# Optimization experiments

Measured on AMD Instinct MI355X. Metric: run time of the kernel, lower is better.

Reference implementation:

```python
import jax, jax.numpy as jnp
import numpy as np

EPS = 1e-5

def _bn(x):
    # BatchNorm (training-mode batch stats, gamma=1, beta=0) over batch+spatial axes
    axes = (0,) + tuple(range(2, x.ndim))
    m = x.mean(axis=axes, keepdims=True)
    v = x.var(axis=axes, keepdims=True)
    return (x - m) / jnp.sqrt(v + EPS)

def _knn(x, k):
    # x: [B, C, N] -> idx [B, N, K] of k nearest neighbors (largest of negative sq dist)
    xt = jnp.swapaxes(x, 1, 2)                      # [B, N, C]
    inner = -2.0 * jnp.einsum('bnc,bmc->bnm', xt, xt)
    xx = jnp.sum(x * x, axis=1)                     # [B, N]
    pdist = -xx[:, :, None] - inner - xx[:, None, :]  # [B, N, N] (negative sq dist)
    return jax.lax.top_k(pdist, k)[1]

def _get_neighbors(x, k):
    # x: [B, C, N] -> edge features [B, 2C, N, K] = concat(neighbor - center, center)
    idx = _knn(x, k)                                # [B, N, K]
    xt = jnp.swapaxes(x, 1, 2)                      # [B, N, C]
    nb = jax.vmap(lambda pts, i: pts[i])(xt, idx)   # [B, N, K, C]
    center = jnp.broadcast_to(xt[:, :, None, :], nb.shape)
    feat = jnp.concatenate([nb - center, center], axis=-1)  # [B, N, K, 2C]
    return jnp.transpose(feat, (0, 3, 1, 2))        # [B, 2C, N, K]

def _sa_layer(x, Wq, Wk, Wt, bt):
    # Faithful SALayerSingleHead: note original computes x_v but never uses it,
    # and uses x @ attention; we match that math exactly. x: [B, C, N]
    xq = jnp.einsum('qc,bcn->bnq', Wq, x)           # [B, N, C/4]
    xk = jnp.einsum('qc,bcn->bqn', Wk, x)           # [B, C/4, N]
    energy = jnp.einsum('bnq,bqm->bnm', xq, xk)     # [B, N, N]
    attn = jax.nn.softmax(energy, axis=-1)
    attn = attn / (1e-6 + attn.sum(axis=1, keepdims=True))
    xr = jnp.einsum('bcn,bnm->bcm', x, attn)        # [B, C, N]
    xr = jax.nn.relu(_bn(jnp.einsum('oc,bcn->bon', Wt, x - xr) + bt[None, :, None]))
    return x + xr

def setup_inputs() -> dict:
    key = jax.random.key(0)
    ks = jax.random.split(key, 12)
    B, N, K = 8, 2048, 32
    s = 0.02
    inp = {
        'x': jax.random.normal(ks[0], (B, 3, N), dtype=jnp.float32),
        'We1': jax.random.normal(ks[1], (64, 6), dtype=jnp.float32) * s,
        'be1': jnp.zeros((64,), jnp.float32),
        'We2': jax.random.normal(ks[2], (64, 128), dtype=jnp.float32) * s,
        'be2': jnp.zeros((64,), jnp.float32),
        'Wq': jax.random.normal(ks[3], (4, 32, 128), dtype=jnp.float32) * s,
        'Wk': jax.random.normal(ks[4], (4, 32, 128), dtype=jnp.float32) * s,
        'Wt': jax.random.normal(ks[5], (4, 128, 128), dtype=jnp.float32) * s,
        'bt': jnp.zeros((4, 128), jnp.float32),
        'Wf': jax.random.normal(ks[6], (1024, 512), dtype=jnp.float32) * s,
        'bf': jnp.zeros((1024,), jnp.float32),
        'Wc1': jax.random.normal(ks[7], (512, 1536), dtype=jnp.float32) * s,
        'bc1': jnp.zeros((512,), jnp.float32),
        'Wc2': jax.random.normal(ks[8], (256, 512), dtype=jnp.float32) * s,
        'bc2': jnp.zeros((256,), jnp.float32),
        'Wc3': jax.random.normal(ks[9], (13, 256), dtype=jnp.float32) * s,
        'bc3': jnp.zeros((13,), jnp.float32),
        'k': K,
    }
    return inp

def reference(x, We1, be1, We2, be2, Wq, Wk, Wt, bt, Wf, bf, Wc1, bc1, Wc2, bc2, Wc3, bc3, k):
    # EdgeConv block 1: xyz -> 64
    e1 = jnp.einsum('oc,bcnk->bonk', We1, _get_neighbors(x, k)) + be1[None, :, None, None]
    f1 = jax.nn.relu(_bn(e1)).max(axis=-1)          # [B, 64, N]
    # EdgeConv block 2: 64 -> 64
    e2 = jnp.einsum('oc,bcnk->bonk', We2, _get_neighbors(f1, k)) + be2[None, :, None, None]
    f2 = jax.nn.relu(_bn(e2)).max(axis=-1)          # [B, 64, N]
    feat = jnp.concatenate([f1, f2], axis=1)        # [B, 128, N]
    # 4 stacked single-head SA layers (PCT offset attention)
    xs = feat
    outs = []
    for i in range(4):
        xs = _sa_layer(xs, Wq[i], Wk[i], Wt[i], bt[i])
        outs.append(xs)
    cat = jnp.concatenate(outs, axis=1)             # [B, 512, N]
    fuse = jax.nn.relu(_bn(jnp.einsum('oc,bcn->bon', Wf, cat) + bf[None, :, None]))  # [B,1024,N]
    g = fuse.max(axis=-1)                           # [B, 1024]
    gl = jnp.broadcast_to(g[:, :, None], (g.shape[0], g.shape[1], cat.shape[2]))
    h = jnp.concatenate([gl, cat], axis=1)          # [B, 1536, N]
    h = jax.nn.relu(_bn(jnp.einsum('oc,bcn->bon', Wc1, h) + bc1[None, :, None]))
    h = jax.nn.relu(_bn(jnp.einsum('oc,bcn->bon', Wc2, h) + bc2[None, :, None]))
    out = jnp.einsum('oc,bcn->bon', Wc3, h) + bc3[None, :, None]  # [B, 13, N]
    return out
```

## Files before the change

### kernel.cpp

```cpp
#include <hip/hip_runtime.h>
#include <math.h>

#define DEV static __device__ __forceinline__

namespace {

constexpr int B = 8;
constexpr int N = 2048;
constexpr int KNN = 32;
constexpr float BNEPS = 1e-5f;

DEV unsigned f2key(float f) {
  unsigned u = __float_as_uint(f);
  return (u & 0x80000000u) ? ~u : (u | 0x80000000u);
}

DEV void atomicMaxFloat(float* addr, float val) {
  if (val >= 0.0f) atomicMax((int*)addr, __float_as_int(val));
  else atomicMin((unsigned int*)addr, (unsigned int)__float_as_int(val));
}

struct SelScratch {
  unsigned hist[256];
  int ss[257];
  int bin;
  int cnt;
};

template <int NK>
DEV unsigned long long radix_select32(const unsigned long long (&keys)[NK], SelScratch& s) {
  const int t = threadIdx.x;
  const int lane = t & 63, wave = t >> 6;
  unsigned long long prefix = 0; unsigned long long T = 0;
  int needed = KNN;
  bool done = false;
  for (int level = 0; level < 8 && !done; ++level) {
    int shift = 56 - 8 * level;
    s.hist[t] = 0;
    __syncthreads();
    unsigned long long maskhi = level ? (~0ull << (64 - 8 * level)) : 0ull;
    #pragma unroll
    for (int j = 0; j < NK; ++j) {
      if ((keys[j] & maskhi) == prefix)
        atomicAdd(&s.hist[(unsigned)(keys[j] >> shift) & 255u], 1u);
    }
    __syncthreads();
    if (wave == 0) {
      unsigned h0 = s.hist[4 * lane], h1 = s.hist[4 * lane + 1], h2 = s.hist[4 * lane + 2], h3 = s.hist[4 * lane + 3];
      unsigned s3 = h3, s2 = h2 + s3, s1 = h1 + s2, s0 = h0 + s1;
      unsigned suf = s0;
      #pragma unroll
      for (int off = 1; off < 64; off <<= 1) {
        unsigned v = __shfl_down(suf, off);
        if (lane + off < 64) suf += v;
      }
      unsigned above = suf - s0;
      s.ss[4 * lane] = (int)(s0 + above); s.ss[4 * lane + 1] = (int)(s1 + above);
      s.ss[4 * lane + 2] = (int)(s2 + above); s.ss[4 * lane + 3] = (int)(s3 + above);
      if (lane == 63) s.ss[256] = 0;
    }
    __syncthreads();
    if (s.ss[t] >= needed && s.ss[t + 1] < needed) s.bin = t;
    __syncthreads();
    int bin = s.bin;
    int hc = (int)s.hist[bin];
    needed -= s.ss[bin + 1];
    prefix |= ((unsigned long long)(unsigned)bin) << shift;
    if (needed == hc) { T = prefix; done = true; }
    __syncthreads();
  }
  return T;
}

template <int NK>
DEV void collect32(const unsigned long long (&keys)[NK], unsigned long long T, SelScratch& s,
                   int* __restrict__ out) {
  if (threadIdx.x == 0) s.cnt = 0;
  __syncthreads();
  #pragma unroll
  for (int j = 0; j < NK; ++j) {
    if (keys[j] >= T) {
      int pos = atomicAdd(&s.cnt, 1);
      out[pos] = (int)~(unsigned)keys[j];
    }
  }
  __syncthreads();
}

__global__ __launch_bounds__(256) void knn1_kernel(const float* __restrict__ x, int* __restrict__ idx) {
  __shared__ SelScratch s;
  __shared__ double cc[3];
  int bn = blockIdx.x, b = bn >> 11, n = bn & (N - 1);
  int t = threadIdx.x;
  const float* xb = x + (size_t)b * 3 * N;
  if (t < 3) cc[t] = (double)xb[(size_t)t * N + n];
  __syncthreads();
  double cx = cc[0], cy = cc[1], cz = cc[2];
  unsigned long long keys[8];
  #pragma unroll
  for (int j = 0; j < 8; ++j) {
    int m = t + 256 * j;
    double dx = (double)xb[m] - cx, dy = (double)xb[N + m] - cy, dz = (double)xb[2 * N + m] - cz;
    double pd = -(dx * dx + dy * dy + dz * dz);
    keys[j] = ((unsigned long long)f2key((float)pd) << 32) | (unsigned)~m;
  }
  __syncthreads();
  unsigned long long T = radix_select32(keys, s);
  collect32(keys, T, s, idx + (size_t)bn * KNN);
}

__global__ __launch_bounds__(256) void edge1_kernel(const float* __restrict__ x, const int* __restrict__ idx,
    const float* __restrict__ We1, const float* __restrict__ be1,
    float* __restrict__ emax, double* __restrict__ epart) {
  __shared__ float Ws[6][65];
  __shared__ float fs[6][33];
  __shared__ float es[64][33];
  __shared__ int  is[KNN];
  int bn = blockIdx.x, b = bn >> 11, n = bn & (N - 1);
  int t = threadIdx.x;
  if (t < KNN) is[t] = idx[(size_t)bn * KNN + t];
  for (int e = t; e < 64 * 6; e += 256) Ws[e % 6][e / 6] = We1[e];
  __syncthreads();
  const float* xb = x + (size_t)b * 3 * N;
  for (int e = t; e < 6 * KNN; e += 256) {
    int c = e >> 5, k = e & 31;
    int m = is[k];
    fs[c][k] = (c < 3) ? (xb[(size_t)c * N + m] - xb[(size_t)c * N + n]) : xb[(size_t)(c - 3) * N + n];
  }
  __syncthreads();
  int k = t & 31, orow = t >> 5;
  float acc[8];
  #pragma unroll
  for (int j = 0; j < 8; ++j) acc[j] = 0.0f;
  #pragma unroll
  for (int c = 0; c < 6; ++c) {
    float fv = fs[c][k];
    #pragma unroll
    for (int j = 0; j < 8; ++j) acc[j] = __fadd_rn(acc[j], __fmul_rn(Ws[c][orow * 8 + j], fv));
  }
  #pragma unroll
  for (int j = 0; j < 8; ++j) es[orow * 8 + j][k] = __fadd_rn(acc[j], be1[orow * 8 + j]);
  __syncthreads();
  if (t < 64) {
    double sum = 0, s2 = 0; float mx = -3.402823466e38f;
    #pragma unroll 8
    for (int kk = 0; kk < KNN; ++kk) {
      float v = es[t][kk]; double dv = (double)v;
      sum += dv; s2 = fma(dv, dv, s2); mx = fmaxf(mx, v);
    }
    emax[((size_t)b * 64 + t) * N + n] = mx;
    epart[(size_t)bn * 128 + t] = sum;
    epart[(size_t)bn * 128 + 64 + t] = s2;
  }
}

__global__ __launch_bounds__(256) void edge_stats_kernel(const double* __restrict__ epart, float* __restrict__ ems) {
  __shared__ double r1[256], r2[256];
  int o = blockIdx.x, t = threadIdx.x;
  double s = 0, s2 = 0;
  for (int i = t; i < B * N; i += 256) { s += epart[(size_t)i * 128 + o]; s2 += epart[(size_t)i * 128 + 64 + o]; }
  r1[t] = s; r2[t] = s2; __syncthreads();
  for (int st = 128; st > 0; st >>= 1) { if (t < st) { r1[t] += r1[t + st]; r2[t] += r2[t + st]; } __syncthreads(); }
  if (t == 0) {
    double cnt = (double)(B * N * KNN);
    double m = r1[0] / cnt, v = r2[0] / cnt - m * m;
    ems[o] = (float)m; ems[64 + o] = (float)v;
  }
}

__global__ __launch_bounds__(256) void edge_finish_kernel(const float* __restrict__ emax, const float* __restrict__ ems,
                                                          float* __restrict__ f, float* __restrict__ ft) {
  size_t i = (size_t)blockIdx.x * 256 + threadIdx.x;
  int c = (int)((i >> 11) & 63);
  float sd = sqrtf(ems[64 + c] + BNEPS);
  float v = (emax[i] - ems[c]) / sd;
  v = v > 0.f ? v : 0.f;
  f[i] = v;
  if (ft) {
    int n = (int)(i & (N - 1)); int b = (int)(i >> 17);
    ft[((size_t)b * N + n) * 64 + c] = v;
  }
}

__global__ __launch_bounds__(256) void xx2_kernel(const float* __restrict__ f1, double* __restrict__ xx2) {
  int i = blockIdx.x * 256 + threadIdx.x;
  int b = i >> 11, n = i & (N - 1);
  const float* p = f1 + (size_t)b * 64 * N + n;
  double s = 0;
  #pragma unroll 16
  for (int c = 0; c < 64; ++c) { double v = (double)p[(size_t)c * N]; s = fma(v, v, s); }
  xx2[i] = s;
}

__global__ __launch_bounds__(256) void knn2_kernel(const float* __restrict__ f1, const float* __restrict__ f1t,
                                                   const double* __restrict__ xx2, int* __restrict__ idx) {
  __shared__ SelScratch s;
  __shared__ double ctr[4][64];
  __shared__ unsigned long long stash[2][8][256];
  int bx = blockIdx.x, b = bx >> 9, n0 = (bx & 511) * 4;
  int t = threadIdx.x;
  { int i = t >> 6, c = t & 63; ctr[i][c] = (double)f1t[((size_t)b * N + n0 + i) * 64 + c]; }
  __syncthreads();
  const float* fb = f1 + (size_t)b * 64 * N;
  const double* xxb = xx2 + (size_t)b * N;
  double xxn0 = xxb[n0], xxn1 = xxb[n0 + 1], xxn2 = xxb[n0 + 2], xxn3 = xxb[n0 + 3];
  int mbase = t * 8;
  double xm[8];
  #pragma unroll
  for (int j = 0; j < 8; ++j) xm[j] = xxb[mbase + j];
  double a[4][8];
  #pragma unroll
  for (int i = 0; i < 4; ++i)
    #pragma unroll
    for (int j = 0; j < 8; ++j) a[i][j] = 0.0;
  #pragma unroll 4
  for (int c = 0; c < 64; ++c) {
    double w0 = ctr[0][c], w1 = ctr[1][c], w2 = ctr[2][c], w3 = ctr[3][c];
    float4 fA = *(const float4*)&fb[(size_t)c * N + mbase];
    float4 fB = *(const float4*)&fb[(size_t)c * N + mbase + 4];
    float fv[8] = {fA.x, fA.y, fA.z, fA.w, fB.x, fB.y, fB.z, fB.w};
    #pragma unroll
    for (int j = 0; j < 8; ++j) {
      double v = (double)fv[j];
      a[0][j] = fma(v, w0, a[0][j]);
      a[1][j] = fma(v, w1, a[1][j]);
      a[2][j] = fma(v, w2, a[2][j]);
      a[3][j] = fma(v, w3, a[3][j]);
    }
  }
  unsigned long long k0[8], k1[8];
  #pragma unroll
  for (int j = 0; j < 8; ++j) {
    unsigned long long lo = (unsigned)~(mbase + j);
    k0[j] = ((unsigned long long)f2key((float)(-xxn0 + 2.0 * a[0][j] - xm[j])) << 32) | lo;
    k1[j] = ((unsigned long long)f2key((float)(-xxn1 + 2.0 * a[1][j] - xm[j])) << 32) | lo;
    stash[0][j][t] = ((unsigned long long)f2key((float)(-xxn2 + 2.0 * a[2][j] - xm[j])) << 32) | lo;
    stash[1][j][t] = ((unsigned long long)f2key((float)(-xxn3 + 2.0 * a[3][j] - xm[j])) << 32) | lo;
  }
  __syncthreads();
  unsigned long long T;
  T = radix_select32(k0, s); collect32(k0, T, s, idx + ((size_t)b * N + n0 + 0) * KNN);
  T = radix_select32(k1, s); collect32(k1, T, s, idx + ((size_t)b * N + n0 + 1) * KNN);
  unsigned long long kk[8];
  #pragma unroll
  for (int j = 0; j < 8; ++j) kk[j] = stash[0][j][t];
  T = radix_select32(kk, s); collect32(kk, T, s, idx + ((size_t)b * N + n0 + 2) * KNN);
  #pragma unroll
  for (int j = 0; j < 8; ++j) kk[j] = stash[1][j][t];
  T = radix_select32(kk, s); collect32(kk, T, s, idx + ((size_t)b * N + n0 + 3) * KNN);
}

__global__ __launch_bounds__(256) void edge2_kernel(const float* __restrict__ f1t, const int* __restrict__ idx,
    const float* __restrict__ We2, const float* __restrict__ be2,
    float* __restrict__ emax, double* __restrict__ epart) {
  __shared__ __align__(16) float smem[8448];
  __shared__ int is[4][32];
  float* Wsb = smem;
  float* fsb = smem + 2176;
  int bx = blockIdx.x;
  int b = bx >> 9, n0 = (bx & 511) * 4;
  int t = threadIdx.x;
  if (t < 128) is[t >> 5][t & 31] = idx[((size_t)b * N + n0 + (t >> 5)) * KNN + (t & 31)];
  int o4 = t & 15, kq = (t >> 4) & 3, p = t >> 6;
  float acc[4][8];
  #pragma unroll
  for (int i = 0; i < 4; ++i)
    #pragma unroll
    for (int j = 0; j < 8; ++j) acc[i][j] = 0.f;
  const float* fbt = f1t + (size_t)b * N * 64;
  for (int cc = 0; cc < 4; ++cc) {
    int c0 = cc * 32;
    __syncthreads();
    for (int e = t; e < 2048; e += 256) { int o = e >> 5, c = e & 31; Wsb[c * 68 + o] = We2[(size_t)o * 128 + c0 + c]; }
    for (int e = t; e < 4096; e += 256) {
      int c = e & 31, kk = (e >> 5) & 31, pp = e >> 10;
      int m = is[pp][kk];
      int cg = c0 + c;
      float v = (cg < 64) ? (fbt[(size_t)m * 64 + cg] - fbt[(size_t)(n0 + pp) * 64 + cg])
                          : fbt[(size_t)(n0 + pp) * 64 + (cg - 64)];
      fsb[(pp * 32 + c) * 36 + kk] = v;
    }
    __syncthreads();
    #pragma unroll 4
    for (int c = 0; c < 32; ++c) {
      float4 w4 = *(const float4*)&Wsb[c * 68 + o4 * 4];
      float4 fa = *(const float4*)&fsb[(p * 32 + c) * 36 + kq * 8];
      float4 fb = *(const float4*)&fsb[(p * 32 + c) * 36 + kq * 8 + 4];
      float wv[4]; *(float4*)wv = w4;
      float fv[8]; *(float4*)fv = fa; *(float4*)(fv + 4) = fb;
      #pragma unroll
      for (int i = 0; i < 4; ++i)
        #pragma unroll
        for (int j = 0; j < 8; ++j) acc[i][j] = fmaf(wv[i], fv[j], acc[i][j]);
    }
  }
  __syncthreads();
  {
    float bv[4]; *(float4*)bv = *(const float4*)&be2[o4 * 4];
    #pragma unroll
    for (int j = 0; j < 8; ++j) {
      int k = kq * 8 + j;
      float4 v4 = make_float4(acc[0][j] + bv[0], acc[1][j] + bv[1], acc[2][j] + bv[2], acc[3][j] + bv[3]);
      *(float4*)&smem[k * 264 + p * 64 + o4 * 4] = v4;
    }
  }
  __syncthreads();
  {
    int pp = t >> 6, o = t & 63;
    double sum = 0, s2 = 0; float mx = -3.402823466e38f;
    #pragma unroll 8
    for (int kk = 0; kk < KNN; ++kk) {
      float v = smem[kk * 264 + pp * 64 + o]; double dv = (double)v;
      sum += dv; s2 = fma(dv, dv, s2); mx = fmaxf(mx, v);
    }
    int n = n0 + pp;
    emax[((size_t)b * 64 + o) * N + n] = mx;
    epart[((size_t)b * N + n) * 128 + o] = sum;
    epart[((size_t)b * N + n) * 128 + 64 + o] = s2;
  }
}

__global__ __launch_bounds__(256) void concat_feat_kernel(const float* __restrict__ f1, const float* __restrict__ f2,
                                                          float* __restrict__ feat) {
  size_t i = (size_t)blockIdx.x * 256 + threadIdx.x;
  int n = (int)(i & (N - 1)); int c = (int)((i >> 11) & 127); int b = (int)(i >> 18);
  feat[i] = (c < 64) ? f1[((size_t)b * 64 + c) * N + n] : f2[((size_t)b * 64 + (c - 64)) * N + n];
}

__global__ __launch_bounds__(256) void sa_qk_kernel(const float* __restrict__ xs, int xs_bstride, int xs_coff,
    const float* __restrict__ Wq, const float* __restrict__ Wk,
    float* __restrict__ xq, float* __restrict__ xk) {
  __shared__ __align__(16) float Ws[32][68];
  __shared__ __align__(16) float vs[32][68];
  int bx = blockIdx.x, b = bx >> 5, n0 = (bx & 31) * 64;
  int t = threadIdx.x;
  int tc = t >> 4, tm = t & 15;
  float acc[4][4];
  #pragma unroll
  for (int i = 0; i < 4; ++i)
    #pragma unroll
    for (int j = 0; j < 4; ++j) acc[i][j] = 0.f;
  for (int cc = 0; cc < 4; ++cc) {
    int c0 = cc * 32;
    __syncthreads();
    for (int e = t; e < 512; e += 256) {
      int o = (e & 15) | ((e >> 7) << 4), cq = (e >> 4) & 7;
      float4 w4 = (o < 32) ? *(const float4*)&Wq[o * 128 + c0 + cq * 4]
                           : *(const float4*)&Wk[(o - 32) * 128 + c0 + cq * 4];
      Ws[cq * 4 + 0][o] = w4.x; Ws[cq * 4 + 1][o] = w4.y; Ws[cq * 4 + 2][o] = w4.z; Ws[cq * 4 + 3][o] = w4.w;
    }
    for (int e = t; e < 512; e += 256) {
      int c = e >> 4, nq = e & 15;
      *(float4*)&vs[c][nq * 4] =
          *(const float4*)&xs[(size_t)b * xs_bstride + (size_t)(xs_coff + c0 + c) * N + n0 + nq * 4];
    }
    __syncthreads();
    #pragma unroll 4
    for (int c = 0; c < 32; ++c) {
      float4 w4 = *(const float4*)&Ws[c][tc * 4];
      float4 v4 = *(const float4*)&vs[c][tm * 4];
      float wv[4] = {w4.x, w4.y, w4.z, w4.w};
      float vv[4] = {v4.x, v4.y, v4.z, v4.w};
      #pragma unroll
      for (int i = 0; i < 4; ++i)
        #pragma unroll
        for (int j = 0; j < 4; ++j) acc[i][j] = fmaf(wv[i], vv[j], acc[i][j]);
    }
  }
  #pragma unroll
  for (int i = 0; i < 4; ++i) {
    int o2 = tc * 4 + i;
    if (o2 < 32) {
      #pragma unroll
      for (int j = 0; j < 4; ++j) {
        int n = n0 + tm * 4 + j;
        xq[((size_t)b * N + n) * 32 + o2] = acc[i][j];
      }
    } else {
      float4 o4 = make_float4(acc[i][0], acc[i][1], acc[i][2], acc[i][3]);
      *(float4*)&xk[((size_t)b * 32 + (o2 - 32)) * N + n0 + tm * 4] = o4;
    }
  }
}

__global__ __launch_bounds__(256) void sa_rowstats_kernel(const float* __restrict__ xq, const float* __restrict__ xk,
    float* __restrict__ rowpart) {
  __shared__ __align__(16) float Qs[32][132];
  __shared__ __align__(16) float Ks[32][68];
  int bx = blockIdx.x;
  int rt = bx & 15, mc = (bx >> 4) & 3, b = bx >> 6;
  int n0 = rt * 128, m0 = mc * 512;
  int t = threadIdx.x, tc = t >> 4, tm = t & 15;
  for (int e = t; e < 1024; e += 256) {
    int r = (e & 15) | ((e >> 7) << 4), q4 = (e >> 4) & 7;
    float4 v = *(const float4*)&xq[((size_t)b * N + n0 + r) * 32 + q4 * 4];
    Qs[q4 * 4 + 0][r] = v.x; Qs[q4 * 4 + 1][r] = v.y; Qs[q4 * 4 + 2][r] = v.z; Qs[q4 * 4 + 3][r] = v.w;
  }
  float rm8[8], rs8[8];
  #pragma unroll
  for (int i = 0; i < 8; ++i) { rm8[i] = -3.402823466e38f; rs8[i] = 0.f; }
  for (int mt = 0; mt < 8; ++mt) {
    int mbase = m0 + mt * 64;
    __syncthreads();
    for (int e = t; e < 512; e += 256) {
      int q = e >> 4, m4 = e & 15;
      *(float4*)&Ks[q][m4 * 4] = *(const float4*)&xk[((size_t)b * 32 + q) * N + mbase + m4 * 4];
    }
    __syncthreads();
    float acc[8][4];
    #pragma unroll
    for (int jc = 0; jc < 8; ++jc)
      #pragma unroll
      for (int jm = 0; jm < 4; ++jm) acc[jc][jm] = 0.f;
    #pragma unroll 4
    for (int c = 0; c < 32; ++c) {
      float4 w0 = *(const float4*)&Qs[c][tc * 4];
      float4 w1 = *(const float4*)&Qs[c][tc * 4 + 64];
      float4 k4 = *(const float4*)&Ks[c][tm * 4];
      float wv[8] = {w0.x, w0.y, w0.z, w0.w, w1.x, w1.y, w1.z, w1.w};
      float kv[4] = {k4.x, k4.y, k4.z, k4.w};
      #pragma unroll
      for (int jc = 0; jc < 8; ++jc)
        #pragma unroll
        for (int jm = 0; jm < 4; ++jm) acc[jc][jm] = fmaf(wv[jc], kv[jm], acc[jc][jm]);
    }
    #pragma unroll
    for (int jc = 0; jc < 8; ++jc) {
      #pragma unroll
      for (int jm = 0; jm < 4; ++jm) {
        float e2 = acc[jc][jm];
        if (e2 > rm8[jc]) { rs8[jc] = rs8[jc] * __expf(rm8[jc] - e2) + 1.0f; rm8[jc] = e2; }
        else rs8[jc] += __expf(e2 - rm8[jc]);
      }
    }
  }
  #pragma unroll
  for (int jc = 0; jc < 8; ++jc) {
    float M = rm8[jc], S = rs8[jc];
    #pragma unroll
    for (int off = 1; off < 16; off <<= 1) {
      float M2 = __shfl_xor(M, off), S2 = __shfl_xor(S, off);
      float mm = fmaxf(M, M2);
      S = S * __expf(M - mm) + S2 * __expf(M2 - mm);
      M = mm;
    }
    if (tm == 0) {
      int r = n0 + tc * 4 + (jc & 3) + (jc >> 2) * 64;
      size_t o = ((size_t)mc * (B * N) + (size_t)b * N + r) * 2;
      rowpart[o] = M; rowpart[o + 1] = S;
    }
  }
}

__global__ void rowstats_merge_kernel(const float* __restrict__ rowpart,
                                      float* __restrict__ rowmax, float* __restrict__ rowsum) {
  int i = blockIdx.x * 256 + threadIdx.x;
  float M = rowpart[(size_t)i * 2], S = rowpart[(size_t)i * 2 + 1];
  #pragma unroll
  for (int mc = 1; mc < 4; ++mc) {
    size_t o = ((size_t)mc * (B * N) + i) * 2;
    float M2 = rowpart[o], S2 = rowpart[o + 1];
    float mm = fmaxf(M, M2);
    S = S * __expf(M - mm) + S2 * __expf(M2 - mm);
    M = mm;
  }
  rowmax[i] = M; rowsum[i] = S;
}

__global__ __launch_bounds__(256) void sa_attny_kernel(const float* __restrict__ xs, int xs_bstride, int xs_coff,
    const float* __restrict__ xq, const float* __restrict__ xk,
    const float* __restrict__ rowmax, const float* __restrict__ rowsum,
    float* __restrict__ Yp, float* __restrict__ cspart) {
  __shared__ __align__(16) float qs[64][36];
  __shared__ float rmv[64], rsv[64];
  __shared__ __align__(16) float Ps[64][68];
  __shared__ __align__(16) float vs[64][132];
  __shared__ float csr[4][64];
  int bx = blockIdx.x;
  int g = bx & 3, m0 = ((bx >> 2) & 31) * 64, b = bx >> 7;
  int t = threadIdx.x;
  int tc = t >> 4, tm = t & 15;
  int tmm = t & 63, tns = t >> 6;
  float kreg[32];
  #pragma unroll
  for (int q = 0; q < 32; ++q) kreg[q] = xk[((size_t)b * 32 + q) * N + m0 + tmm];
  float acc[2][4][4];
  #pragma unroll
  for (int h = 0; h < 2; ++h)
    #pragma unroll
    for (int i = 0; i < 4; ++i)
      #pragma unroll
      for (int j = 0; j < 4; ++j) acc[h][i][j] = 0.f;
  float cs = 0.f;
  const float* xsb = xs + (size_t)b * xs_bstride + (size_t)xs_coff * N;
  for (int nt = g * 8; nt < g * 8 + 8; ++nt) {
    int n0 = nt * 64;
    __syncthreads();
    for (int e = t; e < 512; e += 256) {
      int nn = e >> 3, qq = e & 7;
      *(float4*)&qs[nn][qq * 4] = *(const float4*)&xq[((size_t)b * N + n0 + nn) * 32 + qq * 4];
    }
    if (t < 64) { rmv[t] = rowmax[(size_t)b * N + n0 + t]; rsv[t] = 1.0f / rowsum[(size_t)b * N + n0 + t]; }
    for (int e = t; e < 128 * 64; e += 256) {
      int c = e >> 6, nn = e & 63;
      int M = (nn & 3) | (((nn >> 3) & 7) << 2);
      vs[nn][c ^ M] = xsb[(size_t)c * N + n0 + nn];
    }
    __syncthreads();
    float cp = 0.f;
    #pragma unroll 1
    for (int jj = 0; jj < 16; ++jj) {
      int nn = tns * 16 + jj;
      float ea = 0, eb = 0, ec = 0, ed = 0;
      #pragma unroll
      for (int q4 = 0; q4 < 8; ++q4) {
        float4 qv = *(const float4*)&qs[nn][q4 * 4];
        ea = fmaf(qv.x, kreg[4 * q4 + 0], ea);
        eb = fmaf(qv.y, kreg[4 * q4 + 1], eb);
        ec = fmaf(qv.z, kreg[4 * q4 + 2], ec);
        ed = fmaf(qv.w, kreg[4 * q4 + 3], ed);
      }
      float e2 = (ea + eb) + (ec + ed);
      float p = __expf(e2 - rmv[nn]) * rsv[nn];
      Ps[nn][tmm] = p; cp += p;
    }
    csr[tns][tmm] = cp;
    __syncthreads();
    if (t < 64) cs += csr[0][t] + csr[1][t] + csr[2][t] + csr[3][t];
    #pragma unroll 1
    for (int nn8 = 0; nn8 < 8; ++nn8) {
      int s2x = nn8 << 2;
      int b0 = (tc * 4) ^ s2x;
      #pragma unroll
      for (int kk = 0; kk < 8; ++kk) {
        int nn = nn8 * 8 + kk;
        const int k = kk & 3;
        float4 pa = *(const float4*)&Ps[nn][tm * 4];
        float4 q0 = *(const float4*)&vs[nn][b0];
        float4 q1 = *(const float4*)&vs[nn][64 + b0];
        float pv[4]; *(float4*)pv = pa;
        float xr0[4]; *(float4*)xr0 = q0;
        float xr1[4]; *(float4*)xr1 = q1;
        float xv0[4] = {xr0[0 ^ k], xr0[1 ^ k], xr0[2 ^ k], xr0[3 ^ k]};
        float xv1[4] = {xr1[0 ^ k], xr1[1 ^ k], xr1[2 ^ k], xr1[3 ^ k]};
        #pragma unroll
        for (int i = 0; i < 4; ++i)
          #pragma unroll
          for (int jm = 0; jm < 4; ++jm) {
            acc[0][i][jm] = fmaf(xv0[i], pv[jm], acc[0][i][jm]);
            acc[1][i][jm] = fmaf(xv1[i], pv[jm], acc[1][i][jm]);
          }
      }
    }
  }
  #pragma unroll
  for (int h = 0; h < 2; ++h)
    #pragma unroll
    for (int i = 0; i < 4; ++i) {
      float4 o4 = make_float4(acc[h][i][0], acc[h][i][1], acc[h][i][2], acc[h][i][3]);
      *(float4*)&Yp[(((size_t)g * B + b) * 128 + h * 64 + tc * 4 + i) * N + m0 + tm * 4] = o4;
    }
  if (t < 64) cspart[((size_t)g * B + b) * N + m0 + t] = cs;
}

__global__ __launch_bounds__(256) void sa_wt_kernel(const float* __restrict__ xs, int xs_bstride, int xs_coff,
    const float* __restrict__ Yp, const float* __restrict__ cspart,
    const float* __restrict__ Wt, const float* __restrict__ bt,
    float* __restrict__ tpre) {
  __shared__ __align__(16) float Ws[32][132];
  __shared__ __align__(16) float vs[32][68];
  __shared__ __align__(16) float inv[64];
  int bx = blockIdx.x, b = bx >> 5, n0 = (bx & 31) * 64;
  int t = threadIdx.x;
  if (t < 64) {
    float s = 0;
    #pragma unroll
    for (int g = 0; g < 4; ++g) s += cspart[((size_t)g * B + b) * N + n0 + t];
    inv[t] = 1.0f / (1e-6f + s);
  }
  int tc = t >> 4, tm = t & 15;
  float acc[8][4];
  #pragma unroll
  for (int jc = 0; jc < 8; ++jc)
    #pragma unroll
    for (int jm = 0; jm < 4; ++jm) acc[jc][jm] = 0.f;
  for (int cc = 0; cc < 4; ++cc) {
    int c0 = cc * 32;
    __syncthreads();
    for (int e = t; e < 1024; e += 256) {
      int o = (e & 15) | ((e >> 7) << 4), cq = (e >> 4) & 7;
      float4 w4 = *(const float4*)&Wt[o * 128 + c0 + cq * 4];
      Ws[cq * 4 + 0][o] = w4.x; Ws[cq * 4 + 1][o] = w4.y; Ws[cq * 4 + 2][o] = w4.z; Ws[cq * 4 + 3][o] = w4.w;
    }
    for (int e = t; e < 512; e += 256) {
      int c = e >> 4, nq = e & 15;
      float4 xv = *(const float4*)&xs[(size_t)b * xs_bstride + (size_t)(xs_coff + c0 + c) * N + n0 + nq * 4];
      float4 ys = make_float4(0.f, 0.f, 0.f, 0.f);
      #pragma unroll
      for (int g = 0; g < 4; ++g) {
        float4 yv = *(const float4*)&Yp[(((size_t)g * B + b) * 128 + c0 + c) * N + n0 + nq * 4];
        ys.x += yv.x; ys.y += yv.y; ys.z += yv.z; ys.w += yv.w;
      }
      float4 iv = *(const float4*)&inv[nq * 4];
      float4 r = make_float4(xv.x - ys.x * iv.x, xv.y - ys.y * iv.y, xv.z - ys.z * iv.z, xv.w - ys.w * iv.w);
      *(float4*)&vs[c][nq * 4] = r;
    }
    __syncthreads();
    #pragma unroll 4
    for (int c = 0; c < 32; ++c) {
      float4 w0 = *(const float4*)&Ws[c][tc * 4];
      float4 w1 = *(const float4*)&Ws[c][tc * 4 + 64];
      float4 v4 = *(const float4*)&vs[c][tm * 4];
      float wv[8] = {w0.x, w0.y, w0.z, w0.w, w1.x, w1.y, w1.z, w1.w};
      float vv[4] = {v4.x, v4.y, v4.z, v4.w};
      #pragma unroll
      for (int jc = 0; jc < 8; ++jc)
        #pragma unroll
        for (int jm = 0; jm < 4; ++jm) acc[jc][jm] = fmaf(wv[jc], vv[jm], acc[jc][jm]);
    }
  }
  #pragma unroll
  for (int jc = 0; jc < 8; ++jc) {
    int o2 = tc * 4 + (jc & 3) + (jc >> 2) * 64;
    float bias = bt[o2];
    float4 o4 = make_float4(acc[jc][0] + bias, acc[jc][1] + bias, acc[jc][2] + bias, acc[jc][3] + bias);
    *(float4*)&tpre[((size_t)b * 128 + o2) * N + n0 + tm * 4] = o4;
  }
}

__global__ __launch_bounds__(256) void chanstats_kernel(const float* __restrict__ x, float* __restrict__ ms, int C) {
  __shared__ double r1[256], r2[256];
  int c = blockIdx.x, t = threadIdx.x;
  double s = 0, s2 = 0;
  for (int i = t; i < B * N; i += 256) {
    int b = i >> 11, n = i & (N - 1);
    double v = (double)x[((size_t)b * C + c) * N + n];
    s += v; s2 = fma(v, v, s2);
  }
  r1[t] = s; r2[t] = s2; __syncthreads();
  for (int st = 128; st > 0; st >>= 1) { if (t < st) { r1[t] += r1[t + st]; r2[t] += r2[t + st]; } __syncthreads(); }
  if (t == 0) {
    double cnt = (double)(B * N);
    double m = r1[0] / cnt, v = r2[0] / cnt - m * m;
    ms[c] = (float)m; ms[C + c] = (float)v;
  }
}

__global__ __launch_bounds__(256) void sa_out_kernel(const float* __restrict__ tpre, const float* __restrict__ ms,
    const float* __restrict__ xs, int xs_bstride, int xs_coff, float* __restrict__ cat, int lay) {
  size_t i = (size_t)blockIdx.x * 256 + threadIdx.x;
  int n = (int)(i & (N - 1)); int c = (int)((i >> 11) & 127); int b = (int)(i >> 18);
  float sd = sqrtf(ms[128 + c] + BNEPS);
  float v = (tpre[i] - ms[c]) / sd;
  v = v > 0.f ? v : 0.f;
  float xv = xs[(size_t)b * xs_bstride + (size_t)(xs_coff + c) * N + n];
  cat[((size_t)b * 512 + lay * 128 + c) * N + n] = xv + v;
}

__global__ __launch_bounds__(256) void fuse_kernel(const float* __restrict__ cat, const float* __restrict__ Wf,
    const float* __restrict__ bf, float* __restrict__ fps, float* __restrict__ fps2, float* __restrict__ premax) {
  __shared__ __align__(16) float Ws[32][132];
  __shared__ __align__(16) float vs[32][132];
  int bx = blockIdx.x;
  int b = bx >> 7, o0 = ((bx >> 4) & 7) * 128, ntile = bx & 15, n0 = ntile * 128;
  int part = b * 16 + ntile;
  int t = threadIdx.x, ty = t >> 4, tx = t & 15;
  float acc[8][8];
  #pragma unroll
  for (int jo = 0; jo < 8; ++jo)
    #pragma unroll
    for (int ji = 0; ji < 8; ++ji) acc[jo][ji] = 0.f;
  for (int cc = 0; cc < 16; ++cc) {
    int c0 = cc * 32;
    __syncthreads();
    for (int e = t; e < 1024; e += 256) {
      int o = (e & 15) | ((e >> 7) << 4), cq = (e >> 4) & 7;
      float4 w4 = *(const float4*)&Wf[(size_t)(o0 + o) * 512 + c0 + cq * 4];
      Ws[cq * 4 + 0][o] = w4.x; Ws[cq * 4 + 1][o] = w4.y; Ws[cq * 4 + 2][o] = w4.z; Ws[cq * 4 + 3][o] = w4.w;
    }
    for (int e = t; e < 1024; e += 256) {
      int c = e >> 5, nq = e & 31;
      *(float4*)&vs[c][nq * 4] = *(const float4*)&cat[((size_t)b * 512 + c0 + c) * N + n0 + nq * 4];
    }
    __syncthreads();
    #pragma unroll 4
    for (int c = 0; c < 32; ++c) {
      float4 w0 = *(const float4*)&Ws[c][ty * 4];
      float4 w1 = *(const float4*)&Ws[c][64 + ty * 4];
      float4 v0 = *(const float4*)&vs[c][tx * 4];
      float4 v1 = *(const float4*)&vs[c][64 + tx * 4];
      float wv[8] = {w0.x, w0.y, w0.z, w0.w, w1.x, w1.y, w1.z, w1.w};
      float vv[8] = {v0.x, v0.y, v0.z, v0.w, v1.x, v1.y, v1.z, v1.w};
      #pragma unroll
      for (int jo = 0; jo < 8; ++jo)
        #pragma unroll
        for (int ji = 0; ji < 8; ++ji) acc[jo][ji] = fmaf(wv[jo], vv[ji], acc[jo][ji]);
    }
  }
  #pragma unroll
  for (int jo = 0; jo < 8; ++jo) {
    int o = ty * 4 + (jo & 3) + (jo >> 2) * 64;
    float bias = bf[o0 + o];
    double s = 0, s2 = 0; float mx = -3.402823466e38f;
    #pragma unroll
    for (int ji = 0; ji < 8; ++ji) {
      float v = acc[jo][ji] + bias;
      double dv = (double)v;
      s += dv; s2 = fma(dv, dv, s2); mx = fmaxf(mx, v);
    }
    #pragma unroll
    for (int off = 1; off < 16; off <<= 1) {
      s += __shfl_xor(s, off);
      s2 += __shfl_xor(s2, off);
      mx = fmaxf(mx, __shfl_xor(mx, off));
    }
    if (tx == 0) {
      fps[(size_t)(o0 + o) * 128 + part] = (float)s;
      fps2[(size_t)(o0 + o) * 128 + part] = (float)s2;
      atomicMaxFloat(&premax[(size_t)b * 1024 + o0 + o], mx);
    }
  }
}

__global__ __launch_bounds__(128) void fuse_stats_kernel(const float* __restrict__ fps, const float* __restrict__ fps2,
                                                         float* __restrict__ ms) {
  __shared__ double r1[128], r2[128];
  int o = blockIdx.x, t = threadIdx.x;
  r1[t] = (double)fps[(size_t)o * 128 + t];
  r2[t] = (double)fps2[(size_t)o * 128 + t];
  __syncthreads();
  for (int st = 64; st > 0; st >>= 1) { if (t < st) { r1[t] += r1[t + st]; r2[t] += r2[t + st]; } __syncthreads(); }
  if (t == 0) {
    double cnt = (double)(B * N);
    double m = r1[0] / cnt, v = r2[0] / cnt - m * m;
    ms[o] = (float)m; ms[1024 + o] = (float)v;
  }
}

__global__ void g_kernel(const float* __restrict__ premax, const float* __restrict__ ms, float* __restrict__ g) {
  int i = blockIdx.x * 256 + threadIdx.x;
  int o = i & 1023;
  float sd = sqrtf(ms[1024 + o] + BNEPS);
  float v = (premax[i] - ms[o]) / sd;
  g[i] = v > 0.f ? v : 0.f;
}

__global__ __launch_bounds__(256) void gproj_kernel(const float* __restrict__ Wc1, const float* __restrict__ g,
                                                    float* __restrict__ gproj) {
  int i = blockIdx.x * 256 + threadIdx.x;
  int b = i >> 9, o = i & 511;
  const float* gb = g + (size_t)b * 1024;
  const float* wr = Wc1 + (size_t)o * 1536;
  float s = 0;
  #pragma unroll 8
  for (int c = 0; c < 1024; ++c) s = fmaf(wr[c], gb[c], s);
  gproj[i] = s;
}

__global__ __launch_bounds__(256) void mlp_gemm_kernel(const float* __restrict__ in, int Cin,
    const float* __restrict__ W, int wstride, int wcoff,
    const float* __restrict__ bias, const float* __restrict__ extra, int Cout,
    float* __restrict__ out) {
  __shared__ __align__(16) float Ws[32][132];
  __shared__ __align__(16) float vs[32][132];
  int otiles = Cout >> 7;
  int bx = blockIdx.x;
  int b = bx / (otiles * 16); int rem = bx % (otiles * 16);
  int o0 = (rem >> 4) * 128, n0 = (rem & 15) * 128;
  int t = threadIdx.x, ty = t >> 4, tx = t & 15;
  float acc[8][8];
  #pragma unroll
  for (int jo = 0; jo < 8; ++jo)
    #pragma unroll
    for (int ji = 0; ji < 8; ++ji) acc[jo][ji] = 0.f;
  for (int c0 = 0; c0 < Cin; c0 += 32) {
    __syncthreads();
    for (int e = t; e < 1024; e += 256) {
      int o = (e & 15) | ((e >> 7) << 4), cq = (e >> 4) & 7;
      float4 w4 = *(const float4*)&W[(size_t)(o0 + o) * wstride + wcoff + c0 + cq * 4];
      Ws[cq * 4 + 0][o] = w4.x; Ws[cq * 4 + 1][o] = w4.y; Ws[cq * 4 + 2][o] = w4.z; Ws[cq * 4 + 3][o] = w4.w;
    }
    for (int e = t; e < 1024; e += 256) {
      int c = e >> 5, nq = e & 31;
      *(float4*)&vs[c][nq * 4] = *(const float4*)&in[((size_t)b * Cin + c0 + c) * N + n0 + nq * 4];
    }
    __syncthreads();
    #pragma unroll 4
    for (int c = 0; c < 32; ++c) {
      float4 w0 = *(const float4*)&Ws[c][ty * 4];
      float4 w1 = *(const float4*)&Ws[c][64 + ty * 4];
      float4 v0 = *(const float4*)&vs[c][tx * 4];
      float4 v1 = *(const float4*)&vs[c][64 + tx * 4];
      float wv[8] = {w0.x, w0.y, w0.z, w0.w, w1.x, w1.y, w1.z, w1.w};
      float vv[8] = {v0.x, v0.y, v0.z, v0.w, v1.x, v1.y, v1.z, v1.w};
      #pragma unroll
      for (int jo = 0; jo < 8; ++jo)
        #pragma unroll
        for (int ji = 0; ji < 8; ++ji) acc[jo][ji] = fmaf(wv[jo], vv[ji], acc[jo][ji]);
    }
  }
  #pragma unroll
  for (int jo = 0; jo < 8; ++jo) {
    int o2 = o0 + ty * 4 + (jo & 3) + (jo >> 2) * 64;
    float add = bias[o2] + (extra ? extra[(size_t)b * Cout + o2] : 0.f);
    float4 a0 = make_float4(acc[jo][0] + add, acc[jo][1] + add, acc[jo][2] + add, acc[jo][3] + add);
    float4 a1 = make_float4(acc[jo][4] + add, acc[jo][5] + add, acc[jo][6] + add, acc[jo][7] + add);
    *(float4*)&out[((size_t)b * Cout + o2) * N + n0 + tx * 4] = a0;
    *(float4*)&out[((size_t)b * Cout + o2) * N + n0 + 64 + tx * 4] = a1;
  }
}

__global__ void bnrelu_inplace_kernel(float* __restrict__ x, const float* __restrict__ ms, int C) {
  size_t i = (size_t)blockIdx.x * 256 + threadIdx.x;
  int c = (int)((i >> 11) & (C - 1));
  float sd = sqrtf(ms[C + c] + BNEPS);
  float v = (x[i] - ms[c]) / sd;
  x[i] = v > 0.f ? v : 0.f;
}

__global__ __launch_bounds__(256) void wc3_kernel(const float* __restrict__ h, const float* __restrict__ Wc3,
                                                  const float* __restrict__ bc3, float* __restrict__ out) {
  __shared__ float Ws[13][257];
  int bx = blockIdx.x;
  int b = bx >> 3, n0 = (bx & 7) * 256;
  int t = threadIdx.x;
  for (int e = t; e < 13 * 256; e += 256) { int o = e >> 8, c = e & 255; Ws[o][c] = Wc3[o * 256 + c]; }
  __syncthreads();
  float s[13];
  #pragma unroll
  for (int o = 0; o < 13; ++o) s[o] = 0.f;
  const float* hb = h + (size_t)b * 256 * N + n0 + t;
  #pragma unroll 4
  for (int c = 0; c < 256; ++c) {
    float hv = hb[(size_t)c * N];
    #pragma unroll
    for (int o = 0; o < 13; ++o) s[o] = fmaf(Ws[o][c], hv, s[o]);
  }
  #pragma unroll
  for (int o = 0; o < 13; ++o) out[((size_t)b * 13 + o) * N + n0 + t] = s[o] + bc3[o];
}

__global__ void init_kernel(float* __restrict__ premax) {
  int i = blockIdx.x * 256 + threadIdx.x;
  if (i < 8192) premax[i] = -3.402823466e38f;
}

}

extern "C" void kernel_launch(void* const* d_in, const int* in_sizes, int n_in,
                              void* d_out, int out_size, void* d_ws, size_t ws_size,
                              hipStream_t stream) {
  const float* x   = (const float*)d_in[0];
  const float* We1 = (const float*)d_in[1];
  const float* be1 = (const float*)d_in[2];
  const float* We2 = (const float*)d_in[3];
  const float* be2 = (const float*)d_in[4];
  const float* Wq  = (const float*)d_in[5];
  const float* Wk  = (const float*)d_in[6];
  const float* Wt  = (const float*)d_in[7];
  const float* bt  = (const float*)d_in[8];
  const float* Wf  = (const float*)d_in[9];
  const float* bf  = (const float*)d_in[10];
  const float* Wc1 = (const float*)d_in[11];
  const float* bc1 = (const float*)d_in[12];
  const float* Wc2 = (const float*)d_in[13];
  const float* bc2 = (const float*)d_in[14];
  const float* Wc3 = (const float*)d_in[15];
  const float* bc3 = (const float*)d_in[16];
  float* out = (float*)d_out;

  char* w = (char*)d_ws;
  size_t off = 0;
  auto take = [&](size_t nbytes) { void* p = w + off; off += (nbytes + 255) & ~(size_t)255; return p; };
  int*    idx1   = (int*)   take((size_t)B * N * KNN * 4);
  int*    idx2   = (int*)   take((size_t)B * N * KNN * 4);
  float*  f1     = (float*) take((size_t)B * 64 * N * 4);
  float*  f2     = (float*) take((size_t)B * 64 * N * 4);
  float*  f1t    = (float*) take((size_t)B * N * 64 * 4);
  double* xx2d   = (double*)take((size_t)B * N * 8);
  double* epart  = (double*)take((size_t)B * N * 128 * 8);
  float*  emax   = (float*) take((size_t)B * 64 * N * 4);
  float*  ems    = (float*) take(128 * 4);
  float*  feat   = (float*) take((size_t)B * 128 * N * 4);
  float*  cat    = (float*) take((size_t)B * 512 * N * 4);
  float*  xq     = (float*) take((size_t)B * N * 32 * 4);
  float*  xk     = (float*) take((size_t)B * 32 * N * 4);
  float*  rowmax = (float*) take((size_t)B * N * 4);
  float*  rowsum = (float*) take((size_t)B * N * 4);
  float*  rowpart= (float*) take((size_t)4 * B * N * 2 * 4);
  float*  ubuf   = (float*) take((size_t)B * 256 * N * 4);
  float*  tpre   = ubuf + (size_t)B * 128 * N;
  float*  pre2   = ubuf;
  float*  bnstats= (float*) take(2048 * 4);
  float*  fps    = (float*) take((size_t)1024 * 256 * 4);
  float*  fps2   = (float*) take((size_t)1024 * 256 * 4);
  float*  premax = (float*) take((size_t)B * 1024 * 4);
  float*  gbuf   = (float*) take((size_t)B * 1024 * 4);
  float*  gproj  = (float*) take((size_t)B * 512 * 4);
  float*  pre1   = (float*) take((size_t)B * 512 * N * 4);
  float*  Yp     = pre1;
  float*  cspart = fps;
  (void)ws_size; (void)in_sizes; (void)n_in; (void)out_size;

  init_kernel<<<32, 256, 0, stream>>>(premax);

  knn1_kernel<<<B * N, 256, 0, stream>>>(x, idx1);
  edge1_kernel<<<B * N, 256, 0, stream>>>(x, idx1, We1, be1, emax, epart);
  edge_stats_kernel<<<64, 256, 0, stream>>>(epart, ems);
  edge_finish_kernel<<<B * 64 * N / 256, 256, 0, stream>>>(emax, ems, f1, f1t);

  xx2_kernel<<<B * N / 256, 256, 0, stream>>>(f1, xx2d);
  knn2_kernel<<<B * N / 4, 256, 0, stream>>>(f1, f1t, xx2d, idx2);
  edge2_kernel<<<B * 512, 256, 0, stream>>>(f1t, idx2, We2, be2, emax, epart);
  edge_stats_kernel<<<64, 256, 0, stream>>>(epart, ems);
  edge_finish_kernel<<<B * 64 * N / 256, 256, 0, stream>>>(emax, ems, f2, nullptr);
  concat_feat_kernel<<<B * 128 * N / 256, 256, 0, stream>>>(f1, f2, feat);

  for (int lay = 0; lay < 4; ++lay) {
    const float* xs = lay ? cat : feat;
    int bstride = lay ? 512 * N : 128 * N;
    int coff = lay ? (lay - 1) * 128 : 0;
    sa_qk_kernel<<<B * 32, 256, 0, stream>>>(xs, bstride, coff, Wq + lay * 32 * 128, Wk + lay * 32 * 128, xq, xk);
    sa_rowstats_kernel<<<512, 256, 0, stream>>>(xq, xk, rowpart);
    rowstats_merge_kernel<<<B * N / 256, 256, 0, stream>>>(rowpart, rowmax, rowsum);
    sa_attny_kernel<<<B * 32 * 4, 256, 0, stream>>>(xs, bstride, coff, xq, xk, rowmax, rowsum, Yp, cspart);
    sa_wt_kernel<<<B * 32, 256, 0, stream>>>(xs, bstride, coff, Yp, cspart, Wt + lay * 128 * 128, bt + lay * 128, tpre);
    chanstats_kernel<<<128, 256, 0, stream>>>(tpre, bnstats, 128);
    sa_out_kernel<<<B * 128 * N / 256, 256, 0, stream>>>(tpre, bnstats, xs, bstride, coff, cat, lay);
  }

  fuse_kernel<<<B * 8 * 16, 256, 0, stream>>>(cat, Wf, bf, fps, fps2, premax);
  fuse_stats_kernel<<<1024, 128, 0, stream>>>(fps, fps2, bnstats);
  g_kernel<<<B * 1024 / 256, 256, 0, stream>>>(premax, bnstats, gbuf);

  gproj_kernel<<<B * 512 / 256, 256, 0, stream>>>(Wc1, gbuf, gproj);
  mlp_gemm_kernel<<<B * 4 * 16, 256, 0, stream>>>(cat, 512, Wc1, 1536, 1024, bc1, gproj, 512, pre1);
  chanstats_kernel<<<512, 256, 0, stream>>>(pre1, bnstats, 512);
  bnrelu_inplace_kernel<<<B * 512 * N / 256, 256, 0, stream>>>(pre1, bnstats, 512);

  mlp_gemm_kernel<<<B * 2 * 16, 256, 0, stream>>>(pre1, 512, Wc2, 512, 0, bc2, nullptr, 256, pre2);
  chanstats_kernel<<<256, 256, 0, stream>>>(pre2, bnstats, 256);
  bnrelu_inplace_kernel<<<B * 256 * N / 256, 256, 0, stream>>>(pre2, bnstats, 256);

  wc3_kernel<<<B * 8, 256, 0, stream>>>(pre2, Wc3, bc3, out);
}
```

Measured before the change: 2.351 ms.

## Fuse BatchNorm statistics into GEMM epilogues and BN-ReLU into consumer loads

```diff
diff --git a/kernel.cpp b/kernel.cpp
--- a/kernel.cpp
+++ b/kernel.cpp
@@ -325,6 +325,21 @@
   size_t i = (size_t)blockIdx.x * 256 + threadIdx.x;
   int n = (int)(i & (N - 1)); int c = (int)((i >> 11) & 127); int b = (int)(i >> 18);
   feat[i] = (c < 64) ? f1[((size_t)b * 64 + c) * N + n] : f2[((size_t)b * 64 + (c - 64)) * N + n];
+}
+
+__global__ __launch_bounds__(256) void stats_from_parts_kernel(const float* __restrict__ p1,
+    const float* __restrict__ p2, float* __restrict__ ms, int C, int P) {
+  __shared__ double r1[256], r2[256];
+  int o = blockIdx.x, t = threadIdx.x;
+  double s = 0, s2 = 0;
+  for (int i = t; i < P; i += 256) { s += (double)p1[(size_t)o * P + i]; s2 += (double)p2[(size_t)o * P + i]; }
+  r1[t] = s; r2[t] = s2; __syncthreads();
+  for (int st = 128; st > 0; st >>= 1) { if (t < st) { r1[t] += r1[t + st]; r2[t] += r2[t + st]; } __syncthreads(); }
+  if (t == 0) {
+    double cnt = (double)(B * N);
+    double m = r1[0] / cnt, v = r2[0] / cnt - m * m;
+    ms[o] = (float)m; ms[C + o] = (float)v;
+  }
 }
 
 __global__ __launch_bounds__(256) void sa_qk_kernel(const float* __restrict__ xs, int xs_bstride, int xs_coff,
@@ -566,11 +581,12 @@
 __global__ __launch_bounds__(256) void sa_wt_kernel(const float* __restrict__ xs, int xs_bstride, int xs_coff,
     const float* __restrict__ Yp, const float* __restrict__ cspart,
     const float* __restrict__ Wt, const float* __restrict__ bt,
-    float* __restrict__ tpre) {
+    float* __restrict__ tpre, float* __restrict__ wtps, float* __restrict__ wtps2) {
   __shared__ __align__(16) float Ws[32][132];
   __shared__ __align__(16) float vs[32][68];
   __shared__ __align__(16) float inv[64];
   int bx = blockIdx.x, b = bx >> 5, n0 = (bx & 31) * 64;
+  int part = bx;
   int t = threadIdx.x;
   if (t < 64) {
     float s = 0;
@@ -623,26 +639,21 @@
   for (int jc = 0; jc < 8; ++jc) {
     int o2 = tc * 4 + (jc & 3) + (jc >> 2) * 64;
     float bias = bt[o2];
-    float4 o4 = make_float4(acc[jc][0] + bias, acc[jc][1] + bias, acc[jc][2] + bias, acc[jc][3] + bias);
+    float v0 = acc[jc][0] + bias, v1 = acc[jc][1] + bias, v2 = acc[jc][2] + bias, v3 = acc[jc][3] + bias;
+    float4 o4 = make_float4(v0, v1, v2, v3);
     *(float4*)&tpre[((size_t)b * 128 + o2) * N + n0 + tm * 4] = o4;
-  }
-}
-
-__global__ __launch_bounds__(256) void chanstats_kernel(const float* __restrict__ x, float* __restrict__ ms, int C) {
-  __shared__ double r1[256], r2[256];
-  int c = blockIdx.x, t = threadIdx.x;
-  double s = 0, s2 = 0;
-  for (int i = t; i < B * N; i += 256) {
-    int b = i >> 11, n = i & (N - 1);
-    double v = (double)x[((size_t)b * C + c) * N + n];
-    s += v; s2 = fma(v, v, s2);
-  }
-  r1[t] = s; r2[t] = s2; __syncthreads();
-  for (int st = 128; st > 0; st >>= 1) { if (t < st) { r1[t] += r1[t + st]; r2[t] += r2[t + st]; } __syncthreads(); }
-  if (t == 0) {
-    double cnt = (double)(B * N);
-    double m = r1[0] / cnt, v = r2[0] / cnt - m * m;
-    ms[c] = (float)m; ms[C + c] = (float)v;
+    double s = (double)v0 + (double)v1 + (double)v2 + (double)v3;
+    double s2 = fma((double)v0, (double)v0, fma((double)v1, (double)v1,
+                fma((double)v2, (double)v2, (double)v3 * (double)v3)));
+    #pragma unroll
+    for (int off = 1; off < 16; off <<= 1) {
+      s += __shfl_xor(s, off);
+      s2 += __shfl_xor(s2, off);
+    }
+    if (tm == 0) {
+      wtps[(size_t)o2 * 256 + part] = (float)s;
+      wtps2[(size_t)o2 * 256 + part] = (float)s2;
+    }
   }
 }
 
@@ -719,21 +730,6 @@
       fps2[(size_t)(o0 + o) * 128 + part] = (float)s2;
       atomicMaxFloat(&premax[(size_t)b * 1024 + o0 + o], mx);
     }
-  }
-}
-
-__global__ __launch_bounds__(128) void fuse_stats_kernel(const float* __restrict__ fps, const float* __restrict__ fps2,
-                                                         float* __restrict__ ms) {
-  __shared__ double r1[128], r2[128];
-  int o = blockIdx.x, t = threadIdx.x;
-  r1[t] = (double)fps[(size_t)o * 128 + t];
-  r2[t] = (double)fps2[(size_t)o * 128 + t];
-  __syncthreads();
-  for (int st = 64; st > 0; st >>= 1) { if (t < st) { r1[t] += r1[t + st]; r2[t] += r2[t + st]; } __syncthreads(); }
-  if (t == 0) {
-    double cnt = (double)(B * N);
-    double m = r1[0] / cnt, v = r2[0] / cnt - m * m;
-    ms[o] = (float)m; ms[1024 + o] = (float)v;
   }
 }
 
@@ -760,13 +756,15 @@
 __global__ __launch_bounds__(256) void mlp_gemm_kernel(const float* __restrict__ in, int Cin,
     const float* __restrict__ W, int wstride, int wcoff,
     const float* __restrict__ bias, const float* __restrict__ extra, int Cout,
-    float* __restrict__ out) {
+    float* __restrict__ out, const float* __restrict__ inms,
+    float* __restrict__ ps, float* __restrict__ ps2) {
   __shared__ __align__(16) float Ws[32][132];
   __shared__ __align__(16) float vs[32][132];
   int otiles = Cout >> 7;
   int bx = blockIdx.x;
   int b = bx / (otiles * 16); int rem = bx % (otiles * 16);
   int o0 = (rem >> 4) * 128, n0 = (rem & 15) * 128;
+  int part = b * 16 + (rem & 15);
   int t = threadIdx.x, ty = t >> 4, tx = t & 15;
   float acc[8][8];
   #pragma unroll
@@ -782,7 +780,16 @@
     }
     for (int e = t; e < 1024; e += 256) {
       int c = e >> 5, nq = e & 31;
-      *(float4*)&vs[c][nq * 4] = *(const float4*)&in[((size_t)b * Cin + c0 + c) * N + n0 + nq * 4];
+      float4 v = *(const float4*)&in[((size_t)b * Cin + c0 + c) * N + n0 + nq * 4];
+      if (inms) {
+        float m = inms[c0 + c];
+        float sd = sqrtf(inms[Cin + c0 + c] + BNEPS);
+        v.x = (v.x - m) / sd; v.x = v.x > 0.f ? v.x : 0.f;
+        v.y = (v.y - m) / sd; v.y = v.y > 0.f ? v.y : 0.f;
+        v.z = (v.z - m) / sd; v.z = v.z > 0.f ? v.z : 0.f;
+        v.w = (v.w - m) / sd; v.w = v.w > 0.f ? v.w : 0.f;
+      }
+      *(float4*)&vs[c][nq * 4] = v;
     }
     __syncthreads();
     #pragma unroll 4
@@ -803,28 +810,40 @@
   for (int jo = 0; jo < 8; ++jo) {
     int o2 = o0 + ty * 4 + (jo & 3) + (jo >> 2) * 64;
     float add = bias[o2] + (extra ? extra[(size_t)b * Cout + o2] : 0.f);
-    float4 a0 = make_float4(acc[jo][0] + add, acc[jo][1] + add, acc[jo][2] + add, acc[jo][3] + add);
-    float4 a1 = make_float4(acc[jo][4] + add, acc[jo][5] + add, acc[jo][6] + add, acc[jo][7] + add);
+    float w[8];
+    #pragma unroll
+    for (int ji = 0; ji < 8; ++ji) w[ji] = acc[jo][ji] + add;
+    float4 a0 = make_float4(w[0], w[1], w[2], w[3]);
+    float4 a1 = make_float4(w[4], w[5], w[6], w[7]);
     *(float4*)&out[((size_t)b * Cout + o2) * N + n0 + tx * 4] = a0;
     *(float4*)&out[((size_t)b * Cout + o2) * N + n0 + 64 + tx * 4] = a1;
-  }
-}
-
-__global__ void bnrelu_inplace_kernel(float* __restrict__ x, const float* __restrict__ ms, int C) {
-  size_t i = (size_t)blockIdx.x * 256 + threadIdx.x;
-  int c = (int)((i >> 11) & (C - 1));
-  float sd = sqrtf(ms[C + c] + BNEPS);
-  float v = (x[i] - ms[c]) / sd;
-  x[i] = v > 0.f ? v : 0.f;
+    if (ps) {
+      double s = 0, s2 = 0;
+      #pragma unroll
+      for (int ji = 0; ji < 8; ++ji) { double dv = (double)w[ji]; s += dv; s2 = fma(dv, dv, s2); }
+      #pragma unroll
+      for (int off = 1; off < 16; off <<= 1) {
+        s += __shfl_xor(s, off);
+        s2 += __shfl_xor(s2, off);
+      }
+      if (tx == 0) {
+        ps[(size_t)o2 * 128 + part] = (float)s;
+        ps2[(size_t)o2 * 128 + part] = (float)s2;
+      }
+    }
+  }
 }
 
 __global__ __launch_bounds__(256) void wc3_kernel(const float* __restrict__ h, const float* __restrict__ Wc3,
-                                                  const float* __restrict__ bc3, float* __restrict__ out) {
+                                                  const float* __restrict__ bc3, const float* __restrict__ ms,
+                                                  float* __restrict__ out) {
   __shared__ float Ws[13][257];
+  __shared__ float msm[256], msd[256];
   int bx = blockIdx.x;
   int b = bx >> 3, n0 = (bx & 7) * 256;
   int t = threadIdx.x;
   for (int e = t; e < 13 * 256; e += 256) { int o = e >> 8, c = e & 255; Ws[o][c] = Wc3[o * 256 + c]; }
+  if (t < 256) { msm[t] = ms[t]; msd[t] = sqrtf(ms[256 + t] + BNEPS); }
   __syncthreads();
   float s[13];
   #pragma unroll
@@ -832,7 +851,8 @@
   const float* hb = h + (size_t)b * 256 * N + n0 + t;
   #pragma unroll 4
   for (int c = 0; c < 256; ++c) {
-    float hv = hb[(size_t)c * N];
+    float hv = (hb[(size_t)c * N] - msm[c]) / msd[c];
+    hv = hv > 0.f ? hv : 0.f;
     #pragma unroll
     for (int o = 0; o < 13; ++o) s[o] = fmaf(Ws[o][c], hv, s[o]);
   }
@@ -894,6 +914,10 @@
   float*  bnstats= (float*) take(2048 * 4);
   float*  fps    = (float*) take((size_t)1024 * 256 * 4);
   float*  fps2   = (float*) take((size_t)1024 * 256 * 4);
+  float*  wtps   = (float*) take((size_t)128 * 256 * 4);
+  float*  wtps2  = (float*) take((size_t)128 * 256 * 4);
+  float*  mgps   = (float*) take((size_t)512 * 128 * 4);
+  float*  mgps2  = (float*) take((size_t)512 * 128 * 4);
   float*  premax = (float*) take((size_t)B * 1024 * 4);
   float*  gbuf   = (float*) take((size_t)B * 1024 * 4);
   float*  gproj  = (float*) take((size_t)B * 512 * 4);
@@ -924,23 +948,24 @@
     sa_rowstats_kernel<<<512, 256, 0, stream>>>(xq, xk, rowpart);
     rowstats_merge_kernel<<<B * N / 256, 256, 0, stream>>>(rowpart, rowmax, rowsum);
     sa_attny_kernel<<<B * 32 * 4, 256, 0, stream>>>(xs, bstride, coff, xq, xk, rowmax, rowsum, Yp, cspart);
-    sa_wt_kernel<<<B * 32, 256, 0, stream>>>(xs, bstride, coff, Yp, cspart, Wt + lay * 128 * 128, bt + lay * 128, tpre);
-    chanstats_kernel<<<128, 256, 0, stream>>>(tpre, bnstats, 128);
+    sa_wt_kernel<<<B * 32, 256, 0, stream>>>(xs, bstride, coff, Yp, cspart, Wt + lay * 128 * 128, bt + lay * 128,
+                                             tpre, wtps, wtps2);
+    stats_from_parts_kernel<<<128, 256, 0, stream>>>(wtps, wtps2, bnstats, 128, 256);
     sa_out_kernel<<<B * 128 * N / 256, 256, 0, stream>>>(tpre, bnstats, xs, bstride, coff, cat, lay);
   }
 
   fuse_kernel<<<B * 8 * 16, 256, 0, stream>>>(cat, Wf, bf, fps, fps2, premax);
-  fuse_stats_kernel<<<1024, 128, 0, stream>>>(fps, fps2, bnstats);
+  stats_from_parts_kernel<<<1024, 256, 0, stream>>>(fps, fps2, bnstats, 1024, 128);
   g_kernel<<<B * 1024 / 256, 256, 0, stream>>>(premax, bnstats, gbuf);
 
   gproj_kernel<<<B * 512 / 256, 256, 0, stream>>>(Wc1, gbuf, gproj);
-  mlp_gemm_kernel<<<B * 4 * 16, 256, 0, stream>>>(cat, 512, Wc1, 1536, 1024, bc1, gproj, 512, pre1);
-  chanstats_kernel<<<512, 256, 0, stream>>>(pre1, bnstats, 512);
-  bnrelu_inplace_kernel<<<B * 512 * N / 256, 256, 0, stream>>>(pre1, bnstats, 512);
-
-  mlp_gemm_kernel<<<B * 2 * 16, 256, 0, stream>>>(pre1, 512, Wc2, 512, 0, bc2, nullptr, 256, pre2);
-  chanstats_kernel<<<256, 256, 0, stream>>>(pre2, bnstats, 256);
-  bnrelu_inplace_kernel<<<B * 256 * N / 256, 256, 0, stream>>>(pre2, bnstats, 256);
-
-  wc3_kernel<<<B * 8, 256, 0, stream>>>(pre2, Wc3, bc3, out);
-}
+  mlp_gemm_kernel<<<B * 4 * 16, 256, 0, stream>>>(cat, 512, Wc1, 1536, 1024, bc1, gproj, 512, pre1,
+                                                  nullptr, mgps, mgps2);
+  stats_from_parts_kernel<<<512, 256, 0, stream>>>(mgps, mgps2, bnstats, 512, 128);
+
+  mlp_gemm_kernel<<<B * 2 * 16, 256, 0, stream>>>(pre1, 512, Wc2, 512, 0, bc2, nullptr, 256, pre2,
+                                                  bnstats, mgps, mgps2);
+  stats_from_parts_kernel<<<256, 256, 0, stream>>>(mgps, mgps2, bnstats, 256, 128);
+
+  wc3_kernel<<<B * 8, 256, 0, stream>>>(pre2, Wc3, bc3, bnstats, out);
+}
```

After: 2.300 ms. 2.2% less time.
